# Kernel tuning notes

Measured on AMD Instinct MI355X. Metric: run time of the kernel, lower is better.

## Reference

```python
import jax, jax.numpy as jnp
import numpy as np

M = 16          # num_particles
EPS = 0.006


def setup_inputs() -> dict:
    key = jax.random.key(0)
    k1, k2, k3, k4 = jax.random.split(key, 4)
    B, P, O = 131072, 16, 4  # batch, pred_horizon, obs_horizon
    return {
        "ys_t": jax.random.normal(k1, (B, P, O), dtype=jnp.float32),
        "ys_r_stop": jax.random.normal(k2, (B, P, O), dtype=jnp.float32),
        "w_scale": jax.random.uniform(k3, (B,), dtype=jnp.float32),
        "time_weights": jax.random.uniform(k4, (B,), dtype=jnp.float32),
    }


def _laplace(a, b, ws, D):
    # a,b: [G, M, D]; ws: [G, M] (scale indexed by j, the first particle index)
    d = jnp.linalg.norm(a[:, :, None, :] - b[:, None, :, :], axis=-1)  # [G, M, M]
    d = jnp.maximum(d, EPS)
    return jnp.exp(-ws[:, :, None] * d / D)


def reference(ys_t, ys_r_stop, w_scale, time_weights):
    B = ys_t.shape[0]
    G = B // M
    x = ys_t.reshape(G, M, -1)        # [G, M, D]
    y = ys_r_stop.reshape(G, M, -1)   # [G, M, D]
    D = x.shape[-1]                   # pred_horizon * obs_horizon (dim_normalize)
    ws = w_scale.reshape(G, M)
    tw = time_weights.reshape(G, M)[:, 0]  # [G]
    terms = _laplace(x, x, ws, D) + _laplace(y, y, ws, D) - 2.0 * _laplace(x, y, ws, D)
    group_loss = terms.sum(axis=(1, 2)) * tw / (M * M)  # [G]
    return group_loss.sum() / G
```

## Files before the change

### kernel.cpp

```cpp
#include <hip/hip_runtime.h>


#define EPS_D 0.006f
#define DIMS 64

#define ROT(v, O) __int_as_float(__builtin_amdgcn_update_dpp(              \
        0, __float_as_int(v), 0x120 + (O), 0xF, 0xF, false))

__global__ __launch_bounds__(256, 2)
void imm_loss_kernel(const float* __restrict__ ys_t,
                     const float* __restrict__ ys_r,
                     const float* __restrict__ w_scale,
                     const float* __restrict__ time_w,
                     float* __restrict__ partials)
{
    const int tid  = threadIdx.x;
    const int lane = tid & 63;
    const int wave = tid >> 6;
    const int b    = (blockIdx.x * 4 + wave) * 64 + lane;

    float x[DIMS], y[DIMS];
    const float4* xp = reinterpret_cast<const float4*>(ys_t + (size_t)b * DIMS);
    const float4* yp = reinterpret_cast<const float4*>(ys_r + (size_t)b * DIMS);
    #pragma unroll
    for (int c = 0; c < DIMS / 4; ++c) {
        float4 v = xp[c];
        x[4*c+0] = v.x; x[4*c+1] = v.y; x[4*c+2] = v.z; x[4*c+3] = v.w;
    }
    #pragma unroll
    for (int c = 0; c < DIMS / 4; ++c) {
        float4 v = yp[c];
        y[4*c+0] = v.x; y[4*c+1] = v.y; y[4*c+2] = v.z; y[4*c+3] = v.w;
    }

    const float s_j = w_scale[b] * (1.0f / (float)DIMS);
    const float tw  = time_w[b & ~15];

    float acc = 2.0f * __expf(-s_j * EPS_D);

    {
        float d2 = 0.f;
        #pragma unroll
        for (int d = 0; d < DIMS; ++d) {
            float t = x[d] - y[d];
            d2 = fmaf(t, t, d2);
        }
        float dd = fmaxf(sqrtf(d2), EPS_D);
        acc -= 2.0f * __expf(-s_j * dd);
    }

#define FULL_O(O, W) {                                                     \
        const float s_k = ROT(s_j, O);                                     \
        float dxx = 0.f, dyy = 0.f, dxy = 0.f;                             \
        _Pragma("unroll")                                                  \
        for (int d = 0; d < DIMS; ++d) {                                   \
            float xr = ROT(x[d], O);                                       \
            float yr = ROT(y[d], O);                                       \
            float tx = xr - x[d];  dxx = fmaf(tx, tx, dxx);                \
            float ty = yr - y[d];  dyy = fmaf(ty, ty, dyy);                \
            float tz = yr - x[d];  dxy = fmaf(tz, tz, dxy);                \
        }                                                                  \
        const float ddx = fmaxf(sqrtf(dxx), EPS_D);                        \
        const float ddy = fmaxf(sqrtf(dyy), EPS_D);                        \
        const float ddz = fmaxf(sqrtf(dxy), EPS_D);                        \
        acc += (W) * (__expf(-s_j * ddx) + __expf(-s_k * ddx));            \
        acc += (W) * (__expf(-s_j * ddy) + __expf(-s_k * ddy));            \
        acc -= 2.0f * __expf(-s_j * ddz);                                  \
    }

#define XY_O(O) {                                                          \
        float dxy = 0.f;                                                   \
        _Pragma("unroll")                                                  \
        for (int d = 0; d < DIMS; ++d) {                                   \
            float tz = ROT(y[d], O) - x[d];                                \
            dxy = fmaf(tz, tz, dxy);                                       \
        }                                                                  \
        const float ddz = fmaxf(sqrtf(dxy), EPS_D);                        \
        acc -= 2.0f * __expf(-s_j * ddz);                                  \
    }

    FULL_O(1, 1.0f)
    FULL_O(2, 1.0f)
    FULL_O(3, 1.0f)
    FULL_O(4, 1.0f)
    FULL_O(5, 1.0f)
    FULL_O(6, 1.0f)
    FULL_O(7, 1.0f)
    FULL_O(8, 0.5f)
    XY_O(9)
    XY_O(10)
    XY_O(11)
    XY_O(12)
    XY_O(13)
    XY_O(14)
    XY_O(15)

    float val = acc * tw;
    #pragma unroll
    for (int off = 32; off; off >>= 1)
        val += __shfl_xor(val, off, 64);

    __shared__ float smem[4];
    if (lane == 0) smem[wave] = val;
    __syncthreads();
    if (tid == 0)
        partials[blockIdx.x] = smem[0] + smem[1] + smem[2] + smem[3];
}

__global__ void imm_reduce_kernel(const float* __restrict__ part, int n,
                                  float inv_scale, float* __restrict__ out)
{
    const int tid = threadIdx.x;
    float v = 0.f;
    for (int i = tid; i < n; i += 256) v += part[i];
    #pragma unroll
    for (int off = 32; off; off >>= 1) v += __shfl_xor(v, off, 64);
    __shared__ float s[4];
    if ((tid & 63) == 0) s[tid >> 6] = v;
    __syncthreads();
    if (tid == 0) out[0] = (s[0] + s[1] + s[2] + s[3]) * inv_scale;
}

extern "C" void kernel_launch(void* const* d_in, const int* in_sizes, int n_in,
                              void* d_out, int out_size, void* d_ws, size_t ws_size,
                              hipStream_t stream)
{
    const float* ys_t = (const float*)d_in[0];
    const float* ys_r = (const float*)d_in[1];
    const float* wsc  = (const float*)d_in[2];
    const float* twp  = (const float*)d_in[3];
    float* out      = (float*)d_out;
    float* partials = (float*)d_ws;

    const int B = in_sizes[2];
    const int G = B / 16;
    const int blocks = G / 16;

    imm_loss_kernel<<<blocks, 256, 0, stream>>>(ys_t, ys_r, wsc, twp, partials);

    const float inv_scale = 1.0f / (256.0f * (float)G);
    imm_reduce_kernel<<<1, 256, 0, stream>>>(partials, blocks, inv_scale, out);
}
```

Measured before the change: 119.4 us.

## Compute pairwise distances via norms and Gram dot products with chunked loads

Replaces the direct squared-difference distance loops with the expansion |a|^2+|b|^2-2a·b. Per-lane norms and rotated dot products are accumulated over 16-element chunks of the inputs, and the next chunk is prefetched while the current one is processed. This drops the subtraction per pair and shrinks register use from 128 resident input values to about 64 plus 31 accumulators, which may let the compiler schedule better or avoid spills. The cost is possible cancellation error in the expansion, clamped at zero, and a loop-carried structure that is no longer fully unrolled.

```diff
diff --git a/kernel.cpp b/kernel.cpp
--- a/kernel.cpp
+++ b/kernel.cpp
@@ -3,6 +3,8 @@
 
 #define EPS_D 0.006f
 #define DIMS 64
+#define CH   16
+#define NCH  (DIMS / CH)
 
 #define ROT(v, O) __int_as_float(__builtin_amdgcn_update_dpp(              \
         0, __float_as_int(v), 0x120 + (O), 0xF, 0xF, false))
@@ -19,81 +21,109 @@
     const int wave = tid >> 6;
     const int b    = (blockIdx.x * 4 + wave) * 64 + lane;
 
-    float x[DIMS], y[DIMS];
+    const float s_j = w_scale[b] * (1.0f / (float)DIMS);
+    const float tw  = time_w[b & ~15];
+
     const float4* xp = reinterpret_cast<const float4*>(ys_t + (size_t)b * DIMS);
     const float4* yp = reinterpret_cast<const float4*>(ys_r + (size_t)b * DIMS);
+
+    float nx = 0.f, ny = 0.f, g0 = 0.f;
+    float gxx[8], gyy[8], gxy[8], hxy[7];
     #pragma unroll
-    for (int c = 0; c < DIMS / 4; ++c) {
-        float4 v = xp[c];
-        x[4*c+0] = v.x; x[4*c+1] = v.y; x[4*c+2] = v.z; x[4*c+3] = v.w;
-    }
+    for (int i = 0; i < 8; ++i) { gxx[i] = 0.f; gyy[i] = 0.f; gxy[i] = 0.f; }
     #pragma unroll
-    for (int c = 0; c < DIMS / 4; ++c) {
-        float4 v = yp[c];
-        y[4*c+0] = v.x; y[4*c+1] = v.y; y[4*c+2] = v.z; y[4*c+3] = v.w;
+    for (int i = 0; i < 7; ++i) hxy[i] = 0.f;
+
+    float xc[CH], yc[CH], xn[CH], yn[CH];
+
+    #pragma unroll
+    for (int q = 0; q < CH / 4; ++q) {
+        float4 v = xp[q];
+        xc[4*q+0] = v.x; xc[4*q+1] = v.y; xc[4*q+2] = v.z; xc[4*q+3] = v.w;
+        float4 w = yp[q];
+        yc[4*q+0] = w.x; yc[4*q+1] = w.y; yc[4*q+2] = w.z; yc[4*q+3] = w.w;
     }
 
-    const float s_j = w_scale[b] * (1.0f / (float)DIMS);
-    const float tw  = time_w[b & ~15];
+    #pragma unroll 1
+    for (int c = 0; c < NCH; ++c) {
+        if (c + 1 < NCH) {
+            #pragma unroll
+            for (int q = 0; q < CH / 4; ++q) {
+                float4 v = xp[(c + 1) * (CH / 4) + q];
+                xn[4*q+0] = v.x; xn[4*q+1] = v.y; xn[4*q+2] = v.z; xn[4*q+3] = v.w;
+                float4 w = yp[(c + 1) * (CH / 4) + q];
+                yn[4*q+0] = w.x; yn[4*q+1] = w.y; yn[4*q+2] = w.z; yn[4*q+3] = w.w;
+            }
+        }
+
+        #pragma unroll
+        for (int d = 0; d < CH; ++d) {
+            const float xd = xc[d], yd = yc[d];
+            nx = fmaf(xd, xd, nx);
+            ny = fmaf(yd, yd, ny);
+            g0 = fmaf(xd, yd, g0);
+
+#define ACC_FULL(O) {                                                      \
+            const float xr = ROT(xd, O);                                   \
+            const float yr = ROT(yd, O);                                   \
+            gxx[(O)-1] = fmaf(xr, xd, gxx[(O)-1]);                         \
+            gyy[(O)-1] = fmaf(yr, yd, gyy[(O)-1]);                         \
+            gxy[(O)-1] = fmaf(yr, xd, gxy[(O)-1]); }
+#define ACC_XY(O) {                                                        \
+            const float yr = ROT(yd, O);                                   \
+            hxy[(O)-9] = fmaf(yr, xd, hxy[(O)-9]); }
+
+            ACC_FULL(1) ACC_FULL(2) ACC_FULL(3) ACC_FULL(4)
+            ACC_FULL(5) ACC_FULL(6) ACC_FULL(7) ACC_FULL(8)
+            ACC_XY(9)  ACC_XY(10) ACC_XY(11) ACC_XY(12)
+            ACC_XY(13) ACC_XY(14) ACC_XY(15)
+        }
+
+        if (c + 1 < NCH) {
+            #pragma unroll
+            for (int q = 0; q < CH; ++q) { xc[q] = xn[q]; yc[q] = yn[q]; }
+        }
+    }
 
     float acc = 2.0f * __expf(-s_j * EPS_D);
 
     {
-        float d2 = 0.f;
-        #pragma unroll
-        for (int d = 0; d < DIMS; ++d) {
-            float t = x[d] - y[d];
-            d2 = fmaf(t, t, d2);
-        }
-        float dd = fmaxf(sqrtf(d2), EPS_D);
+        const float d2 = fmaxf(nx + ny - 2.0f * g0, 0.0f);
+        const float dd = fmaxf(sqrtf(d2), EPS_D);
         acc -= 2.0f * __expf(-s_j * dd);
     }
 
-#define FULL_O(O, W) {                                                     \
-        const float s_k = ROT(s_j, O);                                     \
-        float dxx = 0.f, dyy = 0.f, dxy = 0.f;                             \
-        _Pragma("unroll")                                                  \
-        for (int d = 0; d < DIMS; ++d) {                                   \
-            float xr = ROT(x[d], O);                                       \
-            float yr = ROT(y[d], O);                                       \
-            float tx = xr - x[d];  dxx = fmaf(tx, tx, dxx);                \
-            float ty = yr - y[d];  dyy = fmaf(ty, ty, dyy);                \
-            float tz = yr - x[d];  dxy = fmaf(tz, tz, dxy);                \
-        }                                                                  \
-        const float ddx = fmaxf(sqrtf(dxx), EPS_D);                        \
-        const float ddy = fmaxf(sqrtf(dyy), EPS_D);                        \
-        const float ddz = fmaxf(sqrtf(dxy), EPS_D);                        \
-        acc += (W) * (__expf(-s_j * ddx) + __expf(-s_k * ddx));            \
-        acc += (W) * (__expf(-s_j * ddy) + __expf(-s_k * ddy));            \
-        acc -= 2.0f * __expf(-s_j * ddz);                                  \
-    }
+#define FIN_FULL(O, W) {                                                   \
+        const float sk  = ROT(s_j, O);                                     \
+        const float nxr = ROT(nx, O);                                      \
+        const float nyr = ROT(ny, O);                                      \
+        const float ddx = fmaxf(sqrtf(fmaxf(nx + nxr - 2.0f*gxx[(O)-1], 0.f)), EPS_D); \
+        const float ddy = fmaxf(sqrtf(fmaxf(ny + nyr - 2.0f*gyy[(O)-1], 0.f)), EPS_D); \
+        const float ddz = fmaxf(sqrtf(fmaxf(nx + nyr - 2.0f*gxy[(O)-1], 0.f)), EPS_D); \
+        acc += (W) * (__expf(-s_j * ddx) + __expf(-sk * ddx));             \
+        acc += (W) * (__expf(-s_j * ddy) + __expf(-sk * ddy));             \
+        acc -= 2.0f * __expf(-s_j * ddz); }
 
-#define XY_O(O) {                                                          \
-        float dxy = 0.f;                                                   \
-        _Pragma("unroll")                                                  \
-        for (int d = 0; d < DIMS; ++d) {                                   \
-            float tz = ROT(y[d], O) - x[d];                                \
-            dxy = fmaf(tz, tz, dxy);                                       \
-        }                                                                  \
-        const float ddz = fmaxf(sqrtf(dxy), EPS_D);                        \
-        acc -= 2.0f * __expf(-s_j * ddz);                                  \
-    }
+#define FIN_XY(O) {                                                        \
+        const float nyr = ROT(ny, O);                                      \
+        const float ddz = fmaxf(sqrtf(fmaxf(nx + nyr - 2.0f*hxy[(O)-9], 0.f)), EPS_D); \
+        acc -= 2.0f * __expf(-s_j * ddz); }
 
-    FULL_O(1, 1.0f)
-    FULL_O(2, 1.0f)
-    FULL_O(3, 1.0f)
-    FULL_O(4, 1.0f)
-    FULL_O(5, 1.0f)
-    FULL_O(6, 1.0f)
-    FULL_O(7, 1.0f)
-    FULL_O(8, 0.5f)
-    XY_O(9)
-    XY_O(10)
-    XY_O(11)
-    XY_O(12)
-    XY_O(13)
-    XY_O(14)
-    XY_O(15)
+    FIN_FULL(1, 1.0f)
+    FIN_FULL(2, 1.0f)
+    FIN_FULL(3, 1.0f)
+    FIN_FULL(4, 1.0f)
+    FIN_FULL(5, 1.0f)
+    FIN_FULL(6, 1.0f)
+    FIN_FULL(7, 1.0f)
+    FIN_FULL(8, 0.5f)
+    FIN_XY(9)
+    FIN_XY(10)
+    FIN_XY(11)
+    FIN_XY(12)
+    FIN_XY(13)
+    FIN_XY(14)
+    FIN_XY(15)
 
     float val = acc * tw;
     #pragma unroll
```

Result: slower. 303.9 us (+154.6%).
